# Performance work log

Measured on AMD Instinct MI355X. Metric: run time of the kernel, lower is better.

The kernel has to match this reference:

```python
import jax, jax.numpy as jnp
import numpy as np

N = 100_000        # nodes
E = 3_200_000      # edges (avg degree 32)
H = 20             # hidden_channels (forced by forward body)
EH = 64            # edge_hidden_dim
EOUT = 10          # edge_output_dim (forced: 10 + EOUT == H)
THRESHOLD = 10.0


def setup_inputs() -> dict:
    key = jax.random.key(0)
    ks = jax.random.split(key, 12)
    x = jax.random.normal(ks[0], (N, 2, H), dtype=jnp.float32)
    edge_index = jax.random.randint(ks[1], (2, E), 0, N, dtype=jnp.int32)
    # distances must be in (0, threshold]
    edge_attr = jax.random.uniform(ks[2], (E, 1), dtype=jnp.float32, minval=1e-3, maxval=THRESHOLD)
    # module parameters (match torch init distributions: uniform[0,1))
    a = jax.random.uniform(ks[3], (1,), dtype=jnp.float32)
    b = jax.random.uniform(ks[4], (1,), dtype=jnp.float32) + 1.0
    gamma1 = jax.random.uniform(ks[5], (H, H), dtype=jnp.float32)
    gamma2 = jax.random.uniform(ks[6], (H, H), dtype=jnp.float32)
    bias = jax.random.uniform(ks[7], (H,), dtype=jnp.float32)
    # EdgeFeatureMLP2 params: Linear(1->EH), Linear(EH->EOUT)
    W1 = jax.random.normal(ks[8], (1, EH), dtype=jnp.float32)
    b1 = jax.random.normal(ks[9], (EH,), dtype=jnp.float32) * 0.1
    W2 = jax.random.normal(ks[10], (EH, EOUT), dtype=jnp.float32) / np.sqrt(EH)
    b2 = jax.random.normal(ks[11], (EOUT,), dtype=jnp.float32) * 0.1
    return dict(x=x, edge_index=edge_index, edge_attr=edge_attr, a=a, b=b,
                gamma1=gamma1, gamma2=gamma2, bias=bias, W1=W1, b1=b1, W2=W2, b2=b2)


def reference(x, edge_index, edge_attr, a, b, gamma1, gamma2, bias, W1, b1, W2, b2):
    src, dst = edge_index[0], edge_index[1]
    # edge MLP: Linear -> ReLU -> Linear -> ReLU
    h = jax.nn.relu(edge_attr @ W1 + b1)                    # [E, EH]
    mlp_out = jax.nn.relu(h @ W2 + b2)                      # [E, EOUT]
    # one-hot distance bucket: int(d / (threshold/10)), clipped to 9
    idx = jnp.minimum((edge_attr[:, 0] / (THRESHOLD / 10.0)).astype(jnp.int32), 9)
    one_hot = jax.nn.one_hot(idx, 10, dtype=edge_attr.dtype)  # [E, 10]
    comb = jnp.concatenate([one_hot, mlp_out], axis=1)      # [E, 20]
    # w_tilde: per-edge features normalized by the sum over all edges from the source node
    sum_w = jax.ops.segment_sum(comb, src, num_segments=N)  # [N, 20]
    sw = sum_w[src]                                         # [E, 20]
    nz = sw != 0
    w_tilde = jnp.where(nz, comb / jnp.where(nz, sw, 1.0), 0.01)
    # rho weighting: |a*h_j - (1-a)*h_j'|^b, elementwise over the 20-dim slot-0 features
    rho = jnp.abs(a * x[src, 0] - (1.0 - a) * x[dst, 0]) ** b  # [E, 20]
    sum_feat = jax.ops.segment_sum(rho * w_tilde, src, num_segments=N)  # [N, 20]
    # node update: relu(gamma1 @ x_j + gamma2 @ sum_feat_j + bias)
    out0 = jax.nn.relu(x[:, 0] @ gamma1.T + sum_feat @ gamma2.T + bias)  # [N, 20]
    return jnp.stack([out0, sum_feat], axis=1)              # [N, 2, 20]
```

## Files before the change

kernel.cpp:

```cpp
#include <hip/hip_runtime.h>

#define NN 100000
#define NE 3200000
#define HD 20
#define EHD 64
#define EOUTD 10
#define TBINS 4096

#define EPB 2048
#define NBLKS1 1563
#define NBINS1 256
#define N1 (NBINS1 * NBLKS1)
#define NBUCK 196
#define WIN 4096
#define WPB 6
#define NWIN (NBUCK * WPB)
#define N2 (NBUCK * 512 * WPB)
#define KMASK 0x1FFFF

__global__ void scan1_kernel(int* __restrict__ data, int* __restrict__ bsum, int n) {
    __shared__ int s[1024];
    int t = threadIdx.x;
    int i = blockIdx.x * 1024 + t;
    int v = (i < n) ? data[i] : 0;
    s[t] = v;
    __syncthreads();
    for (int off = 1; off < 1024; off <<= 1) {
        int add = (t >= off) ? s[t - off] : 0;
        __syncthreads();
        s[t] += add;
        __syncthreads();
    }
    if (i < n) data[i] = s[t] - v;
    if (t == 1023) bsum[blockIdx.x] = s[t];
}

__global__ void scan3f_kernel(int* __restrict__ data, const int* __restrict__ bsum,
                              int nb, int n) {
    __shared__ int s[1024];
    int t = threadIdx.x;
    int v = (t < nb) ? bsum[t] : 0;
    s[t] = v;
    __syncthreads();
    for (int off = 1; off < 1024; off <<= 1) {
        int add = (t >= off) ? s[t - off] : 0;
        __syncthreads();
        s[t] += add;
        __syncthreads();
    }
    __syncthreads();
    int i = blockIdx.x * 1024 + t;
    if (i < n) data[i] += s[i >> 10] - ((i >> 10) < nb ? bsum[i >> 10] : 0);
}

__global__ void scan3bf_kernel(int* __restrict__ data, const int* __restrict__ bsum,
                               int nb, int* __restrict__ offsets) {
    __shared__ int s[1024];
    int t = threadIdx.x;
    int v = (t < nb) ? bsum[t] : 0;
    s[t] = v;
    __syncthreads();
    for (int off = 1; off < 1024; off <<= 1) {
        int add = (t >= off) ? s[t - off] : 0;
        __syncthreads();
        s[t] += add;
        __syncthreads();
    }
    __syncthreads();
    int i = blockIdx.x * 1024 + t;
    if (i >= N2) return;
    int blk = i >> 10;
    int vv = data[i] + s[blk] - (blk < nb ? bsum[blk] : 0);
    data[i] = vv;
    if (i % WPB == 0) {
        int nbidx = i / WPB;
        if (nbidx <= NN) offsets[nbidx] = vv;
    }
}

__global__ void scatter1_kernel(const int* __restrict__ ei,
                                const float* __restrict__ ea,
                                const int* __restrict__ counts1s,
                                int2* __restrict__ pk1) {
    __shared__ int2 rec[EPB];
    __shared__ int2 srt[EPB];
    __shared__ unsigned char bin8[EPB];
    __shared__ unsigned char bin8s[EPB];
    __shared__ int hh[NBINS1];
    __shared__ int hbase[NBINS1];
    int t = threadIdx.x;
    int blk = blockIdx.x;
    int base = blk * EPB;
    int n = NE - base; if (n > EPB) n = EPB;

    if (t < NBINS1) hh[t] = 0;
    __syncthreads();

    for (int j = t; j < n; j += 512) {
        int e = base + j;
        int src = ei[e];
        int b = src >> 9;
        int2 pk;
        pk.x = ei[NE + e] | ((src & 511) << 17);
        pk.y = __float_as_int(ea[e]);
        rec[j] = pk;
        bin8[j] = (unsigned char)b;
        atomicAdd(&hh[b], 1);
    }
    __syncthreads();

    int orig = (t < NBINS1) ? hh[t] : 0;
    if (t < NBINS1) hbase[t] = orig;
    __syncthreads();
    for (int off = 1; off < NBINS1; off <<= 1) {
        int add = (t < NBINS1 && t >= off) ? hbase[t - off] : 0;
        __syncthreads();
        if (t < NBINS1) hbase[t] += add;
        __syncthreads();
    }
    if (t < NBINS1) {
        hbase[t] -= orig;
        hh[t] = hbase[t];
    }
    __syncthreads();

    for (int j = t; j < n; j += 512) {
        int b = bin8[j];
        int pos = atomicAdd(&hh[b], 1);
        srt[pos] = rec[j];
        bin8s[pos] = (unsigned char)b;
    }
    __syncthreads();

    for (int j = t; j < n; j += 512) {
        int b = bin8s[j];
        int gpos = counts1s[b * NBLKS1 + blk] + (j - hbase[b]);
        pk1[gpos] = srt[j];
    }
}

__global__ void hist2_kernel(const int2* __restrict__ pk1,
                             const int* __restrict__ counts1s,
                             int* __restrict__ M2) {
    __shared__ int h[512];
    int t = threadIdx.x;
    h[t] = 0; h[t + 256] = 0;
    __syncthreads();
    int b = blockIdx.x / WPB, w = blockIdx.x % WPB;
    int bstart = counts1s[b * NBLKS1];
    int bend;
    if (b + 1 < NBINS1) bend = counts1s[(b + 1) * NBLKS1];
    else bend = NE;
    int start = bstart + w * WIN;
    int end = (start + WIN < bend) ? (start + WIN) : bend;
    for (int i = start + t; i < end; i += 256)
        atomicAdd(&h[(pk1[i].x >> 17) & 511], 1);
    __syncthreads();
    M2[((b * 512) + t) * WPB + w]       = h[t];
    M2[((b * 512) + t + 256) * WPB + w] = h[t + 256];
}

__global__ void scatter2_kernel(const int2* __restrict__ pk1,
                                const int* __restrict__ counts1s,
                                const int* __restrict__ M2s,
                                int2* __restrict__ csr_pk) {
    __shared__ int cur[512];
    int t = threadIdx.x;
    int b = blockIdx.x / WPB, w = blockIdx.x % WPB;
    cur[t]       = M2s[((b * 512) + t) * WPB + w];
    cur[t + 256] = M2s[((b * 512) + t + 256) * WPB + w];
    __syncthreads();
    int bstart = counts1s[b * NBLKS1];
    int bend;
    if (b + 1 < NBINS1) bend = counts1s[(b + 1) * NBLKS1];
    else bend = NE;
    int start = bstart + w * WIN;
    int end = (start + WIN < bend) ? (start + WIN) : bend;
    for (int i = start + t; i < end; i += 256) {
        int2 pk = pk1[i];
        int pos = atomicAdd(&cur[(pk.x >> 17) & 511], 1);
        float d = __int_as_float(pk.y);
        int idx = (int)d; if (idx > 9) idx = 9;
        float u = d * ((float)TBINS / 10.0f);
        int ti = (int)u; if (ti > TBINS - 1) ti = TBINS - 1;
        float fr = u - (float)ti;
        int fr16 = (int)(fr * 65536.0f); if (fr16 > 65535) fr16 = 65535;
        pk.x &= KMASK;
        pk.y = fr16 | (ti << 16) | (idx << 28);
        csr_pk[pos] = pk;
    }
}

#define XBLK ((NN * 10 + 255) / 256)
__global__ void prep_kernel(const float* __restrict__ W1,
                            const float* __restrict__ b1,
                            const float* __restrict__ W2,
                            const float* __restrict__ b2,
                            const float* __restrict__ x,
                            const int* __restrict__ ei,
                            unsigned short* __restrict__ tab,
                            int* __restrict__ xbf2,
                            int* __restrict__ counts1) {
    const int TBLK = (TBINS + 255) / 256;
    auto bf16 = [](float f) -> unsigned int {
        unsigned int u = __float_as_uint(f);
        return (u + 0x7fffu + ((u >> 16) & 1u)) >> 16;
    };
    if (blockIdx.x < TBLK) {
        int i = blockIdx.x * 256 + threadIdx.x;
        if (i >= TBINS) return;
        float m0[EOUTD], m1[EOUTD];
        float d0 = (float)i * (10.0f / (float)TBINS);
        float d1 = (float)(i + 1) * (10.0f / (float)TBINS);
        #pragma unroll
        for (int j = 0; j < EOUTD; ++j) { m0[j] = b2[j]; m1[j] = b2[j]; }
        for (int k = 0; k < EHD; ++k) {
            float h0 = fmaxf(fmaf(d0, W1[k], b1[k]), 0.0f);
            float h1 = fmaxf(fmaf(d1, W1[k], b1[k]), 0.0f);
            #pragma unroll
            for (int j = 0; j < EOUTD; ++j) {
                m0[j] = fmaf(h0, W2[k * EOUTD + j], m0[j]);
                m1[j] = fmaf(h1, W2[k * EOUTD + j], m1[j]);
            }
        }
        unsigned short* row = tab + (size_t)i * 32;
        #pragma unroll
        for (int j = 0; j < EOUTD; ++j) {
            row[2 * j]     = (unsigned short)bf16(m0[j]);
            row[2 * j + 1] = (unsigned short)bf16(m1[j] - m0[j]);
        }
        #pragma unroll
        for (int j = 20; j < 32; ++j) row[j] = 0;
    } else if (blockIdx.x < TBLK + XBLK) {
        int t = (blockIdx.x - TBLK) * 256 + threadIdx.x;
        if (t >= NN * 10) return;
        int node = t / 10;
        int k = t - node * 10;
        xbf2[t] = (int)(bf16(x[(size_t)node * 2 * HD + k])
                        | (bf16(x[(size_t)node * 2 * HD + k + 10]) << 16));
    } else {
        __shared__ int h[NBINS1];
        int t = threadIdx.x;
        int blk = blockIdx.x - TBLK - XBLK;
        h[t] = 0;
        __syncthreads();
        int base = blk * EPB;
        for (int j = t; j < EPB; j += 256) {
            int e = base + j;
            if (e < NE) atomicAdd(&h[ei[e] >> 9], 1);
        }
        __syncthreads();
        counts1[t * NBLKS1 + blk] = h[t];
    }
}

__launch_bounds__(256)
__global__ void node_kernel(const int* __restrict__ offsets,
                            const int2* __restrict__ csr_pk,
                            const float* __restrict__ x,
                            const int* __restrict__ xbf2,
                            const unsigned short* __restrict__ tab,
                            const float* __restrict__ pa,
                            const float* __restrict__ pb,
                            const float* __restrict__ g1,
                            const float* __restrict__ g2,
                            const float* __restrict__ bias,
                            float* __restrict__ out) {
    int tid  = threadIdx.x;
    int wave = tid >> 6;
    int lane = tid & 63;
    int sub  = lane / 10;
    int fk   = lane - sub * 10;
    int node = blockIdx.x * 24 + wave * 6 + sub;
    bool active = (sub < 6) && (node < NN);

    float a = pa[0], bb = pb[0];
    float oma = 1.0f - a;

    int off0 = 0, deg = 0;
    float xs_lo = 0.0f, xs_hi = 0.0f, axs_lo = 0.0f, axs_hi = 0.0f;
    if (active) {
        off0 = offsets[node];
        deg  = offsets[node + 1] - off0;
        xs_lo = x[(size_t)node * 2 * HD + fk];
        xs_hi = x[(size_t)node * 2 * HD + fk + 10];
        axs_lo = a * xs_lo;
        axs_hi = a * xs_hi;
    }

    float S0a = 0.0f, S1a = 0.0f, Sra = 0.0f;
    float S0b = 0.0f, S1b = 0.0f, Srb = 0.0f;

    auto process = [&](int dst, int dy) {
        int ti  = (dy >> 16) & 0xFFF;
        int idx = (dy >> 28) & 0xF;
        float fr = (float)(dy & 0xFFFF) * (1.0f / 65536.0f);
        unsigned int xw = (unsigned int)xbf2[(size_t)(unsigned int)dst * 10 + fk];
        unsigned int tv = *(const unsigned int*)(tab + (((size_t)ti) << 5) + fk * 2);
        float xd_lo = __uint_as_float(xw << 16);
        float xd_hi = __uint_as_float(xw & 0xffff0000u);
        float t0 = fmaf(-oma, xd_lo, axs_lo);
        float t1 = fmaf(-oma, xd_hi, axs_hi);
        float r0 = (t0 != 0.0f)
            ? __builtin_amdgcn_exp2f(bb * __builtin_amdgcn_logf(fabsf(t0))) : 0.0f;
        float r1 = (t1 != 0.0f)
            ? __builtin_amdgcn_exp2f(bb * __builtin_amdgcn_logf(fabsf(t1))) : 0.0f;
        Sra += r0; Srb += r1;
        float c0 = (fk == idx) ? 1.0f : 0.0f;
        float val = __uint_as_float(tv << 16);
        float del = __uint_as_float(tv & 0xffff0000u);
        float c1 = fmaxf(fmaf(fr, del, val), 0.0f);
        S0a += c0; S1a = fmaf(r0, c0, S1a);
        S0b += c1; S1b = fmaf(r1, c1, S1b);
    };

    for (int base = 0; base < deg; base += 10) {
        int nchunk = deg - base; if (nchunk > 10) nchunk = 10;
        int idxc = off0 + base + ((fk < nchunk) ? fk : (nchunk - 1));
        int2 pk = csr_pk[idxc];
        int dstv = pk.x, dbits = pk.y;
        int jj = 0;
        for (; jj + 1 < nchunk; jj += 2) {
            int dA = __shfl(dstv, sub * 10 + jj, 64);
            int bA = __shfl(dbits, sub * 10 + jj, 64);
            int dB = __shfl(dstv, sub * 10 + jj + 1, 64);
            int bB = __shfl(dbits, sub * 10 + jj + 1, 64);
            process(dA, bA);
            process(dB, bB);
        }
        if (jj < nchunk) {
            int dA = __shfl(dstv, sub * 10 + jj, 64);
            int bA = __shfl(dbits, sub * 10 + jj, 64);
            process(dA, bA);
        }
    }

    float sf_lo = (S0a != 0.0f) ? (S1a / S0a) : (0.01f * Sra);
    float sf_hi = (S0b != 0.0f) ? (S1b / S0b) : (0.01f * Srb);

    if (active) {
        float acc0 = bias[fk];
        float acc1 = bias[fk + 10];
        const float* g1r0 = g1 + fk * HD;
        const float* g1r1 = g1 + (fk + 10) * HD;
        const float* g2r0 = g2 + fk * HD;
        const float* g2r1 = g2 + (fk + 10) * HD;
        #pragma unroll
        for (int j = 0; j < 10; ++j) {
            int sl = sub * 10 + j;
            float xj  = __shfl(xs_lo, sl, 64);
            float xj1 = __shfl(xs_hi, sl, 64);
            float sj  = __shfl(sf_lo, sl, 64);
            float sj1 = __shfl(sf_hi, sl, 64);
            acc0 = fmaf(xj, g1r0[j], acc0);  acc0 = fmaf(xj1, g1r0[j + 10], acc0);
            acc0 = fmaf(sj, g2r0[j], acc0);  acc0 = fmaf(sj1, g2r0[j + 10], acc0);
            acc1 = fmaf(xj, g1r1[j], acc1);  acc1 = fmaf(xj1, g1r1[j + 10], acc1);
            acc1 = fmaf(sj, g2r1[j], acc1);  acc1 = fmaf(sj1, g2r1[j + 10], acc1);
        }
        float* op = out + (size_t)node * 2 * HD;
        op[fk]          = fmaxf(acc0, 0.0f);
        op[fk + 10]     = fmaxf(acc1, 0.0f);
        op[HD + fk]     = sf_lo;
        op[HD + fk + 10] = sf_hi;
    }
}

extern "C" void kernel_launch(void* const* d_in, const int* in_sizes, int n_in,
                              void* d_out, int out_size, void* d_ws, size_t ws_size,
                              hipStream_t stream) {
    const float* x    = (const float*)d_in[0];
    const int*   ei   = (const int*)d_in[1];
    const float* ea   = (const float*)d_in[2];
    const float* pa   = (const float*)d_in[3];
    const float* pb   = (const float*)d_in[4];
    const float* g1   = (const float*)d_in[5];
    const float* g2   = (const float*)d_in[6];
    const float* bias = (const float*)d_in[7];
    const float* W1   = (const float*)d_in[8];
    const float* b1   = (const float*)d_in[9];
    const float* W2   = (const float*)d_in[10];
    const float* b2   = (const float*)d_in[11];
    float* out = (float*)d_out;

    char* ws = (char*)d_ws;
    int*   counts1 = (int*)ws;     ws += ((size_t)N1 * 4 + 127) / 128 * 128;
    int*   bsum1   = (int*)ws;     ws += (1024 * 4 + 127) / 128 * 128;
    int*   M2      = (int*)ws;     ws += ((size_t)N2 * 4 + 127) / 128 * 128;
    int*   bsum2   = (int*)ws;     ws += (1024 * 4 + 127) / 128 * 128;
    int*   offsets = (int*)ws;     ws += ((size_t)(NN + 1) * 4 + 127) / 128 * 128;
    int2*  pk1     = (int2*)ws;    ws += (size_t)NE * 8;
    int2*  csr_pk  = (int2*)ws;    ws += (size_t)NE * 8;
    unsigned short* tab = (unsigned short*)ws;   ws += ((size_t)TBINS * 32 * 2 + 127) / 128 * 128;
    int*   xbf2    = (int*)ws;     ws += ((size_t)NN * 10 * 4 + 127) / 128 * 128;

    const int TBLK = (TBINS + 255) / 256;
    prep_kernel<<<TBLK + XBLK + NBLKS1, 256, 0, stream>>>(W1, b1, W2, b2, x, ei,
                                                          tab, xbf2, counts1);

    const int nb1 = (N1 + 1023) / 1024;
    scan1_kernel<<<nb1, 1024, 0, stream>>>(counts1, bsum1, N1);
    scan3f_kernel<<<nb1, 1024, 0, stream>>>(counts1, bsum1, nb1, N1);
    scatter1_kernel<<<NBLKS1, 512, 0, stream>>>(ei, ea, counts1, pk1);

    const int nb2 = (N2 + 1023) / 1024;
    hist2_kernel<<<NWIN, 256, 0, stream>>>(pk1, counts1, M2);
    scan1_kernel<<<nb2, 1024, 0, stream>>>(M2, bsum2, N2);
    scan3bf_kernel<<<nb2, 1024, 0, stream>>>(M2, bsum2, nb2, offsets);
    scatter2_kernel<<<NWIN, 256, 0, stream>>>(pk1, counts1, M2, csr_pk);

    node_kernel<<<(NN + 23) / 24, 256, 0, stream>>>(offsets, csr_pk, x, xbf2, tab,
                                                    pa, pb, g1, g2, bias, out);
}
```

Baseline: 168.0 us.

## Fuse second-pass histogram, scan and scatter into one per-bucket kernel

Replaces the second radix pass (histogram kernel, two-level global scan, scatter kernel) with a single kernel. One 1024-thread block per bucket builds the 512-bin histogram, scans it in shared memory, writes the CSR offsets and scatters the edges. This removes three kernel launches and the M2 count array round trip through global memory. In exchange it launches only 196 blocks, fewer than the CU count, and each block processes a whole bucket serially, so some parallelism is lost.

```diff
diff --git a/kernel.cpp b/kernel.cpp
--- a/kernel.cpp
+++ b/kernel.cpp
@@ -12,10 +12,6 @@
 #define NBINS1 256
 #define N1 (NBINS1 * NBLKS1)
 #define NBUCK 196
-#define WIN 4096
-#define WPB 6
-#define NWIN (NBUCK * WPB)
-#define N2 (NBUCK * 512 * WPB)
 #define KMASK 0x1FFFF
 
 __global__ void scan1_kernel(int* __restrict__ data, int* __restrict__ bsum, int n) {
@@ -51,31 +47,6 @@
     __syncthreads();
     int i = blockIdx.x * 1024 + t;
     if (i < n) data[i] += s[i >> 10] - ((i >> 10) < nb ? bsum[i >> 10] : 0);
-}
-
-__global__ void scan3bf_kernel(int* __restrict__ data, const int* __restrict__ bsum,
-                               int nb, int* __restrict__ offsets) {
-    __shared__ int s[1024];
-    int t = threadIdx.x;
-    int v = (t < nb) ? bsum[t] : 0;
-    s[t] = v;
-    __syncthreads();
-    for (int off = 1; off < 1024; off <<= 1) {
-        int add = (t >= off) ? s[t - off] : 0;
-        __syncthreads();
-        s[t] += add;
-        __syncthreads();
-    }
-    __syncthreads();
-    int i = blockIdx.x * 1024 + t;
-    if (i >= N2) return;
-    int blk = i >> 10;
-    int vv = data[i] + s[blk] - (blk < nb ? bsum[blk] : 0);
-    data[i] = vv;
-    if (i % WPB == 0) {
-        int nbidx = i / WPB;
-        if (nbidx <= NN) offsets[nbidx] = vv;
-    }
 }
 
 __global__ void scatter1_kernel(const int* __restrict__ ei,
@@ -139,46 +110,40 @@
     }
 }
 
-__global__ void hist2_kernel(const int2* __restrict__ pk1,
+__global__ void pass2_kernel(const int2* __restrict__ pk1,
                              const int* __restrict__ counts1s,
-                             int* __restrict__ M2) {
+                             int* __restrict__ offsets,
+                             int2* __restrict__ csr_pk) {
     __shared__ int h[512];
+    __shared__ int hb[512];
     int t = threadIdx.x;
-    h[t] = 0; h[t + 256] = 0;
-    __syncthreads();
-    int b = blockIdx.x / WPB, w = blockIdx.x % WPB;
+    int b = blockIdx.x;
+    if (t < 512) h[t] = 0;
+    __syncthreads();
     int bstart = counts1s[b * NBLKS1];
-    int bend;
-    if (b + 1 < NBINS1) bend = counts1s[(b + 1) * NBLKS1];
-    else bend = NE;
-    int start = bstart + w * WIN;
-    int end = (start + WIN < bend) ? (start + WIN) : bend;
-    for (int i = start + t; i < end; i += 256)
+    int bend   = counts1s[(b + 1) * NBLKS1];
+    for (int i = bstart + t; i < bend; i += 1024)
         atomicAdd(&h[(pk1[i].x >> 17) & 511], 1);
     __syncthreads();
-    M2[((b * 512) + t) * WPB + w]       = h[t];
-    M2[((b * 512) + t + 256) * WPB + w] = h[t + 256];
-}
-
-__global__ void scatter2_kernel(const int2* __restrict__ pk1,
-                                const int* __restrict__ counts1s,
-                                const int* __restrict__ M2s,
-                                int2* __restrict__ csr_pk) {
-    __shared__ int cur[512];
-    int t = threadIdx.x;
-    int b = blockIdx.x / WPB, w = blockIdx.x % WPB;
-    cur[t]       = M2s[((b * 512) + t) * WPB + w];
-    cur[t + 256] = M2s[((b * 512) + t + 256) * WPB + w];
-    __syncthreads();
-    int bstart = counts1s[b * NBLKS1];
-    int bend;
-    if (b + 1 < NBINS1) bend = counts1s[(b + 1) * NBLKS1];
-    else bend = NE;
-    int start = bstart + w * WIN;
-    int end = (start + WIN < bend) ? (start + WIN) : bend;
-    for (int i = start + t; i < end; i += 256) {
+    int orig = (t < 512) ? h[t] : 0;
+    if (t < 512) hb[t] = orig;
+    __syncthreads();
+    for (int off = 1; off < 512; off <<= 1) {
+        int add = (t < 512 && t >= off) ? hb[t - off] : 0;
+        __syncthreads();
+        if (t < 512) hb[t] += add;
+        __syncthreads();
+    }
+    if (t < 512) {
+        hb[t] -= orig;
+        h[t] = bstart + hb[t];
+        int node = b * 512 + t;
+        if (node <= NN) offsets[node] = bstart + hb[t];
+    }
+    __syncthreads();
+    for (int i = bstart + t; i < bend; i += 1024) {
         int2 pk = pk1[i];
-        int pos = atomicAdd(&cur[(pk.x >> 17) & 511], 1);
+        int pos = atomicAdd(&h[(pk.x >> 17) & 511], 1);
         float d = __int_as_float(pk.y);
         int idx = (int)d; if (idx > 9) idx = 9;
         float u = d * ((float)TBINS / 10.0f);
@@ -385,8 +350,6 @@
     char* ws = (char*)d_ws;
     int*   counts1 = (int*)ws;     ws += ((size_t)N1 * 4 + 127) / 128 * 128;
     int*   bsum1   = (int*)ws;     ws += (1024 * 4 + 127) / 128 * 128;
-    int*   M2      = (int*)ws;     ws += ((size_t)N2 * 4 + 127) / 128 * 128;
-    int*   bsum2   = (int*)ws;     ws += (1024 * 4 + 127) / 128 * 128;
     int*   offsets = (int*)ws;     ws += ((size_t)(NN + 1) * 4 + 127) / 128 * 128;
     int2*  pk1     = (int2*)ws;    ws += (size_t)NE * 8;
     int2*  csr_pk  = (int2*)ws;    ws += (size_t)NE * 8;
@@ -402,11 +365,7 @@
     scan3f_kernel<<<nb1, 1024, 0, stream>>>(counts1, bsum1, nb1, N1);
     scatter1_kernel<<<NBLKS1, 512, 0, stream>>>(ei, ea, counts1, pk1);
 
-    const int nb2 = (N2 + 1023) / 1024;
-    hist2_kernel<<<NWIN, 256, 0, stream>>>(pk1, counts1, M2);
-    scan1_kernel<<<nb2, 1024, 0, stream>>>(M2, bsum2, N2);
-    scan3bf_kernel<<<nb2, 1024, 0, stream>>>(M2, bsum2, nb2, offsets);
-    scatter2_kernel<<<NWIN, 256, 0, stream>>>(pk1, counts1, M2, csr_pk);
+    pass2_kernel<<<NBUCK, 1024, 0, stream>>>(pk1, counts1, offsets, csr_pk);
 
     node_kernel<<<(NN + 23) / 24, 256, 0, stream>>>(offsets, csr_pk, x, xbf2, tab,
                                                     pa, pb, g1, g2, bias, out);
```

After: 139.9 us. 1.2x faster.
